# Kernel optimization log

Hardware: AMD Instinct MI355X
Metric: run time of the kernel (lower is better)

Reference implementation:

```python
import jax, jax.numpy as jnp
import numpy as np

D = 256; DFFN = 1024; H = 8; NLVL = 4; NPNT = 4; HD = D // H
BS = 4; NQ = 100; NPTS = 25
SPATIAL = [(128, 128), (64, 64), (32, 32), (16, 16)]
LEN_IN = sum(h * w for h, w in SPATIAL)


def _ln(x, g, b, eps=1e-5):
    m = x.mean(-1, keepdims=True)
    v = ((x - m) ** 2).mean(-1, keepdims=True)
    return (x - m) * jax.lax.rsqrt(v + eps) * g + b


def _mha(q, k, v, w_in, b_in, w_out, b_out):
    # torch nn.MultiheadAttention math, batch-first layout [B,S,D]
    B, Sq, _ = q.shape; Sk = k.shape[1]
    wq, wk, wv = jnp.split(w_in, 3, 0); bq, bk, bv = jnp.split(b_in, 3)
    qh = (q @ wq.T + bq).reshape(B, Sq, H, HD).transpose(0, 2, 1, 3)
    kh = (k @ wk.T + bk).reshape(B, Sk, H, HD).transpose(0, 2, 1, 3)
    vh = (v @ wv.T + bv).reshape(B, Sk, H, HD).transpose(0, 2, 1, 3)
    a = jax.nn.softmax(jnp.einsum('bhqd,bhkd->bhqk', qh, kh) * (1.0 / float(np.sqrt(HD))), -1)
    o = jnp.einsum('bhqk,bhkd->bhqd', a, vh).transpose(0, 2, 1, 3).reshape(B, Sq, D)
    return o @ w_out.T + b_out


def _msdeform(query, ref, src, off_w, off_b, aw_w, aw_b, val_w, val_b, out_w, out_b):
    # MSDeformAttn: per-query multi-level bilinear sampling + weighted aggregation
    bs, Lq, _ = query.shape
    value = (src @ val_w.T + val_b).reshape(bs, LEN_IN, H, HD)
    off = (query @ off_w.T + off_b).reshape(bs, Lq, H, NLVL, NPNT, 2)
    aw = jax.nn.softmax((query @ aw_w.T + aw_b).reshape(bs, Lq, H, NLVL * NPNT), -1)
    aw = aw.reshape(bs, Lq, H, NLVL, NPNT)
    norm = jnp.array([[w, h] for h, w in SPATIAL], jnp.float32)  # (W,H) per level
    loc = ref[:, :, None, :, None, :] + off / norm[None, None, None, :, None, :]
    out = jnp.zeros((bs, H, Lq, HD), query.dtype)
    start = 0
    for l, (hh, ww) in enumerate(SPATIAL):
        v_l = value[:, start:start + hh * ww].transpose(0, 2, 1, 3)  # [bs,H,hw,HD]
        start += hh * ww
        # grid_sample align_corners=False pixel coords: loc*size - 0.5
        x = (loc[:, :, :, l, :, 0] * ww - 0.5).transpose(0, 2, 1, 3).reshape(bs, H, Lq * NPNT)
        y = (loc[:, :, :, l, :, 1] * hh - 0.5).transpose(0, 2, 1, 3).reshape(bs, H, Lq * NPNT)
        x0 = jnp.floor(x); y0 = jnp.floor(y); wx = x - x0; wy = y - y0
        x0i = x0.astype(jnp.int32); y0i = y0.astype(jnp.int32); x1i = x0i + 1; y1i = y0i + 1
        def g(xi, yi):
            valid = ((xi >= 0) & (xi < ww) & (yi >= 0) & (yi < hh)).astype(query.dtype)
            idx = jnp.clip(yi, 0, hh - 1) * ww + jnp.clip(xi, 0, ww - 1)
            return jnp.take_along_axis(v_l, idx[..., None], axis=2) * valid[..., None]
        s = (g(x0i, y0i) * ((1 - wx) * (1 - wy))[..., None]
             + g(x1i, y0i) * (wx * (1 - wy))[..., None]
             + g(x0i, y1i) * ((1 - wx) * wy)[..., None]
             + g(x1i, y1i) * (wx * wy)[..., None])
        s = s.reshape(bs, H, Lq, NPNT, HD)
        out = out + (s * aw[:, :, :, l].transpose(0, 2, 1, 3)[..., None]).sum(3)
    return out.transpose(0, 2, 1, 3).reshape(bs, Lq, D) @ out_w.T + out_b


def _fwd(tgt, query_pos, reference_points, src,
         w_in_intra, b_in_intra, w_out_intra, b_out_intra, g_norm_intra, b_norm_intra,
         w_in_inter, b_in_inter, w_out_inter, b_out_inter, g_norm_inter, b_norm_inter,
         off_w, off_b, aw_w, aw_b, val_w, val_b, co_w, co_b, g_norm_cross, b_norm_cross,
         lin1_w, lin1_b, lin2_w, lin2_b, g_norm3, b_norm3):
    bs, nq, npts, d = tgt.shape
    # intra-instance self-attention (over control points)
    q = (tgt + query_pos).reshape(bs * nq, npts, d)
    t2 = _mha(q, q, tgt.reshape(bs * nq, npts, d), w_in_intra, b_in_intra, w_out_intra, b_out_intra)
    tgt = _ln(tgt + t2.reshape(bs, nq, npts, d), g_norm_intra, b_norm_intra)
    # inter-instance self-attention (over queries), no pos embed per source code
    ti = tgt.transpose(0, 2, 1, 3).reshape(bs * npts, nq, d)
    t2 = _mha(ti, ti, ti, w_in_inter, b_in_inter, w_out_inter, b_out_inter)
    ti = _ln(ti + t2, g_norm_inter, b_norm_inter).reshape(bs, npts, nq, d).transpose(0, 2, 1, 3)
    # deformable cross-attention
    ref = jnp.broadcast_to(reference_points[:, :, None], (bs, nq, npts, NLVL, 2)).reshape(bs, nq * npts, NLVL, 2)
    qc = (ti + query_pos).reshape(bs, nq * npts, d)
    t2 = _msdeform(qc, ref, src, off_w, off_b, aw_w, aw_b, val_w, val_b, co_w, co_b).reshape(bs, nq, npts, d)
    tgt = _ln(ti + t2, g_norm_cross, b_norm_cross)
    # FFN
    ff = jax.nn.relu(tgt @ lin1_w.T + lin1_b) @ lin2_w.T + lin2_b
    return _ln(tgt + ff, g_norm3, b_norm3)


def setup_inputs() -> dict:
    key = jax.random.key(0)
    ki = iter(jax.random.split(key, 40))
    def rn(shape, sc=0.02):
        return jax.random.normal(next(ki), shape, jnp.float32) * sc
    inp = dict(
        tgt=jax.random.normal(next(ki), (BS, NQ, NPTS, D), jnp.float32),
        query_pos=jax.random.normal(next(ki), (BS, NQ, NPTS, D), jnp.float32),
        reference_points=jax.random.uniform(next(ki), (BS, NQ, NLVL, 2), jnp.float32),
        src=jax.random.normal(next(ki), (BS, LEN_IN, D), jnp.float32),
        w_in_intra=rn((3 * D, D)), b_in_intra=jnp.zeros((3 * D,), jnp.float32),
        w_out_intra=rn((D, D)), b_out_intra=jnp.zeros((D,), jnp.float32),
        g_norm_intra=jnp.ones((D,), jnp.float32), b_norm_intra=jnp.zeros((D,), jnp.float32),
        w_in_inter=rn((3 * D, D)), b_in_inter=jnp.zeros((3 * D,), jnp.float32),
        w_out_inter=rn((D, D)), b_out_inter=jnp.zeros((D,), jnp.float32),
        g_norm_inter=jnp.ones((D,), jnp.float32), b_norm_inter=jnp.zeros((D,), jnp.float32),
        off_w=rn((H * NLVL * NPNT * 2, D), 0.001), off_b=rn((H * NLVL * NPNT * 2,), 0.5),
        aw_w=rn((H * NLVL * NPNT, D)), aw_b=jnp.zeros((H * NLVL * NPNT,), jnp.float32),
        val_w=rn((D, D)), val_b=jnp.zeros((D,), jnp.float32),
        co_w=rn((D, D)), co_b=jnp.zeros((D,), jnp.float32),
        g_norm_cross=jnp.ones((D,), jnp.float32), b_norm_cross=jnp.zeros((D,), jnp.float32),
        lin1_w=rn((DFFN, D)), lin1_b=jnp.zeros((DFFN,), jnp.float32),
        lin2_w=rn((D, DFFN)), lin2_b=jnp.zeros((D,), jnp.float32),
        g_norm3=jnp.ones((D,), jnp.float32), b_norm3=jnp.zeros((D,), jnp.float32),
        src_spatial_shapes=jnp.array(SPATIAL, jnp.int32),
        level_start_index=jnp.array(np.cumsum([0] + [h * w for h, w in SPATIAL[:-1]]), jnp.int32),
    )
    return inp


def reference(tgt, query_pos, reference_points, src,
              w_in_intra, b_in_intra, w_out_intra, b_out_intra, g_norm_intra, b_norm_intra,
              w_in_inter, b_in_inter, w_out_inter, b_out_inter, g_norm_inter, b_norm_inter,
              off_w, off_b, aw_w, aw_b, val_w, val_b, co_w, co_b, g_norm_cross, b_norm_cross,
              lin1_w, lin1_b, lin2_w, lin2_b, g_norm3, b_norm3,
              src_spatial_shapes, level_start_index):
    # spatial shapes / level starts are compile-time constants (SPATIAL); args kept for signature parity
    return _fwd(tgt, query_pos, reference_points, src,
                w_in_intra, b_in_intra, w_out_intra, b_out_intra, g_norm_intra, b_norm_intra,
                w_in_inter, b_in_inter, w_out_inter, b_out_inter, g_norm_inter, b_norm_inter,
                off_w, off_b, aw_w, aw_b, val_w, val_b, co_w, co_b, g_norm_cross, b_norm_cross,
                lin1_w, lin1_b, lin2_w, lin2_b, g_norm3, b_norm3)
```

## Files before the change

### kernel.cpp

```cpp
#include <hip/hip_runtime.h>
#include <math.h>

#define DMODEL 256
#define HEADS  8
#define HDIM   32
#define BS     4
#define NQ     100
#define NPTS   25
#define LQ     2500
#define M10K   10000
#define LEN_IN 21760
#define MVAL   87040

typedef float f32x4 __attribute__((ext_vector_type(4)));
typedef short s16x8 __attribute__((ext_vector_type(8)));
typedef unsigned short u16;

static __device__ __forceinline__ short f2bf(float f) {
    unsigned u = __builtin_bit_cast(unsigned, f);
    u = (u + 0x7fffu + ((u >> 16) & 1u)) >> 16;
    return (short)u;
}
static __device__ __forceinline__ unsigned pack2(float lo, float hi) {
    return (unsigned)(u16)f2bf(lo) | ((unsigned)(u16)f2bf(hi) << 16);
}
static __device__ __forceinline__ float bf_lo(unsigned u) {
    return __builtin_bit_cast(float, u << 16);
}
static __device__ __forceinline__ float bf_hi(unsigned u) {
    return __builtin_bit_cast(float, u & 0xffff0000u);
}

#define LDSK   40
#define LDSK64 72

__global__ __launch_bounds__(256) void convert_weights_kernel(
    const float* __restrict__ s0, const float* __restrict__ s1,
    const float* __restrict__ s2, const float* __restrict__ s3,
    const float* __restrict__ s4, const float* __restrict__ s5,
    const float* __restrict__ s6, const float* __restrict__ s7,
    const float* __restrict__ s8, const float* __restrict__ s9,
    u16* __restrict__ dst)
{
    int t8 = (blockIdx.x * 256 + threadIdx.x) * 8;
    if (t8 >= 1277952) return;
    const float* s; int base;
    if      (t8 <  196608) { s = s0; base = 0;       }
    else if (t8 <  262144) { s = s1; base = 196608;  }
    else if (t8 <  458752) { s = s2; base = 262144;  }
    else if (t8 <  524288) { s = s3; base = 458752;  }
    else if (t8 <  589824) { s = s4; base = 524288;  }
    else if (t8 <  622592) { s = s5; base = 589824;  }
    else if (t8 <  688128) { s = s6; base = 622592;  }
    else if (t8 <  753664) { s = s7; base = 688128;  }
    else if (t8 < 1015808) { s = s8; base = 753664;  }
    else                   { s = s9; base = 1015808; }
    const float* p = s + (t8 - base);
    float4 a = *(const float4*)p;
    float4 b = *(const float4*)(p + 4);
    s16x8 v;
    v[0]=f2bf(a.x); v[1]=f2bf(a.y); v[2]=f2bf(a.z); v[3]=f2bf(a.w);
    v[4]=f2bf(b.x); v[5]=f2bf(b.y); v[6]=f2bf(b.z); v[7]=f2bf(b.w);
    *(s16x8*)(dst + t8) = v;
}

__global__ __launch_bounds__(256) void add_convert_kernel(
    const float* __restrict__ a, const float* __restrict__ b,
    u16* __restrict__ xb, u16* __restrict__ ab, int n8)
{
    int i = blockIdx.x * 256 + threadIdx.x;
    if (i >= n8) return;
    size_t o = (size_t)i * 8;
    float4 a0 = *(const float4*)(a + o);
    float4 a1 = *(const float4*)(a + o + 4);
    if (ab) {
        s16x8 v;
        v[0]=f2bf(a0.x); v[1]=f2bf(a0.y); v[2]=f2bf(a0.z); v[3]=f2bf(a0.w);
        v[4]=f2bf(a1.x); v[5]=f2bf(a1.y); v[6]=f2bf(a1.z); v[7]=f2bf(a1.w);
        *(s16x8*)(ab + o) = v;
    }
    if (b) {
        float4 b0 = *(const float4*)(b + o);
        float4 b1 = *(const float4*)(b + o + 4);
        a0.x += b0.x; a0.y += b0.y; a0.z += b0.z; a0.w += b0.w;
        a1.x += b1.x; a1.y += b1.y; a1.z += b1.z; a1.w += b1.w;
    }
    s16x8 v;
    v[0]=f2bf(a0.x); v[1]=f2bf(a0.y); v[2]=f2bf(a0.z); v[3]=f2bf(a0.w);
    v[4]=f2bf(a1.x); v[5]=f2bf(a1.y); v[6]=f2bf(a1.z); v[7]=f2bf(a1.w);
    *(s16x8*)(xb + o) = v;
}

__global__ __launch_bounds__(256) void gemm_mfma_kernel(
    const u16* __restrict__ A, int lda,
    const u16* __restrict__ W, int K,
    const float* __restrict__ bias,
    void* __restrict__ Cv, int ldc,
    int M, int relu, int out_bf16)
{
    __shared__ short As[64 * LDSK64];
    __shared__ short Ws[64 * LDSK64];

    const int tid = threadIdx.x;
    const int m0 = blockIdx.y * 64, n0 = blockIdx.x * 64;
    const int srow = tid >> 2;
    const int sk = (tid & 3) * 16;
    const int wave = tid >> 6;
    const int wm = wave & 1, wn = wave >> 1;
    const int lane = tid & 63;
    const int lrow = lane & 15;
    const int kq = lane >> 4;

    const int gm = m0 + srow;
    const u16* aptr = A + (size_t)gm * lda + sk;
    const u16* wptr = W + (size_t)(n0 + srow) * K + sk;

    f32x4 acc[2][2];
#pragma unroll
    for (int i = 0; i < 2; ++i)
#pragma unroll
        for (int j = 0; j < 2; ++j) acc[i][j] = (f32x4)(0.f);

    s16x8 a0 = (s16x8)0, a1 = (s16x8)0, w0, w1;
    if (gm < M) { a0 = *(const s16x8*)aptr; a1 = *(const s16x8*)(aptr + 8); }
    w0 = *(const s16x8*)wptr; w1 = *(const s16x8*)(wptr + 8);

    for (int k0 = 0; k0 < K; k0 += 64) {
        *(s16x8*)&As[srow * LDSK64 + sk]     = a0;
        *(s16x8*)&As[srow * LDSK64 + sk + 8] = a1;
        *(s16x8*)&Ws[srow * LDSK64 + sk]     = w0;
        *(s16x8*)&Ws[srow * LDSK64 + sk + 8] = w1;
        __syncthreads();
        if (k0 + 64 < K) {
            if (gm < M) {
                a0 = *(const s16x8*)(aptr + k0 + 64);
                a1 = *(const s16x8*)(aptr + k0 + 72);
            }
            w0 = *(const s16x8*)(wptr + k0 + 64);
            w1 = *(const s16x8*)(wptr + k0 + 72);
        }

#pragma unroll
        for (int s = 0; s < 2; ++s) {
            s16x8 af[2], bfv[2];
#pragma unroll
            for (int i = 0; i < 2; ++i)
                af[i] = *(const s16x8*)&As[(wm * 32 + i * 16 + lrow) * LDSK64 + s * 32 + kq * 8];
#pragma unroll
            for (int j = 0; j < 2; ++j)
                bfv[j] = *(const s16x8*)&Ws[(wn * 32 + j * 16 + lrow) * LDSK64 + s * 32 + kq * 8];
#pragma unroll
            for (int i = 0; i < 2; ++i)
#pragma unroll
                for (int j = 0; j < 2; ++j)
                    acc[i][j] = __builtin_amdgcn_mfma_f32_16x16x32_bf16(af[i], bfv[j], acc[i][j], 0, 0, 0);
        }
        __syncthreads();
    }

#pragma unroll
    for (int i = 0; i < 2; ++i)
#pragma unroll
        for (int j = 0; j < 2; ++j) {
            int col = n0 + wn * 32 + j * 16 + lrow;
            float bv = bias[col];
#pragma unroll
            for (int reg = 0; reg < 4; ++reg) {
                int gmo = m0 + wm * 32 + i * 16 + kq * 4 + reg;
                if (gmo < M) {
                    float v = acc[i][j][reg] + bv;
                    if (relu) v = fmaxf(v, 0.f);
                    if (out_bf16)
                        ((u16*)Cv)[(size_t)gmo * ldc + col] = (u16)f2bf(v);
                    else
                        ((float*)Cv)[(size_t)gmo * ldc + col] = v;
                }
            }
        }
}

__global__ __launch_bounds__(256) void gemm_mfma128_kernel(
    const u16* __restrict__ A, int lda,
    const u16* __restrict__ W, int K,
    const float* __restrict__ bias,
    void* __restrict__ Cv, int ldc,
    int M, int relu, int out_bf16)
{
    __shared__ short As[128 * LDSK];
    __shared__ short Ws[128 * LDSK];

    const int tid = threadIdx.x;
    const int m0 = blockIdx.y * 128, n0 = blockIdx.x * 128;

    const int srow = tid >> 1;
    const int sk = (tid & 1) * 16;

    const int wave = tid >> 6;
    const int wm = wave & 1, wn = wave >> 1;
    const int lane = tid & 63;
    const int lrow = lane & 15;
    const int kq = lane >> 4;

    const int gm = m0 + srow;
    const u16* aptr = A + (size_t)gm * lda + sk;
    const u16* wptr = W + (size_t)(n0 + srow) * K + sk;

    f32x4 acc[4][4];
#pragma unroll
    for (int i = 0; i < 4; ++i)
#pragma unroll
        for (int j = 0; j < 4; ++j) acc[i][j] = (f32x4)(0.f);

    s16x8 a0 = (s16x8)0, a1 = (s16x8)0, w0, w1;
    if (gm < M) { a0 = *(const s16x8*)aptr; a1 = *(const s16x8*)(aptr + 8); }
    w0 = *(const s16x8*)wptr; w1 = *(const s16x8*)(wptr + 8);

    for (int k0 = 0; k0 < K; k0 += 32) {
        *(s16x8*)&As[srow * LDSK + sk]     = a0;
        *(s16x8*)&As[srow * LDSK + sk + 8] = a1;
        *(s16x8*)&Ws[srow * LDSK + sk]     = w0;
        *(s16x8*)&Ws[srow * LDSK + sk + 8] = w1;
        __syncthreads();
        if (k0 + 32 < K) {
            if (gm < M) {
                a0 = *(const s16x8*)(aptr + k0 + 32);
                a1 = *(const s16x8*)(aptr + k0 + 40);
            }
            w0 = *(const s16x8*)(wptr + k0 + 32);
            w1 = *(const s16x8*)(wptr + k0 + 40);
        }

        s16x8 af[4], bfv[4];
#pragma unroll
        for (int i = 0; i < 4; ++i)
            af[i] = *(const s16x8*)&As[(wm * 64 + i * 16 + lrow) * LDSK + kq * 8];
#pragma unroll
        for (int j = 0; j < 4; ++j)
            bfv[j] = *(const s16x8*)&Ws[(wn * 64 + j * 16 + lrow) * LDSK + kq * 8];
#pragma unroll
        for (int i = 0; i < 4; ++i)
#pragma unroll
            for (int j = 0; j < 4; ++j)
                acc[i][j] = __builtin_amdgcn_mfma_f32_16x16x32_bf16(af[i], bfv[j], acc[i][j], 0, 0, 0);
        __syncthreads();
    }

#pragma unroll
    for (int i = 0; i < 4; ++i)
#pragma unroll
        for (int j = 0; j < 4; ++j) {
            int col = n0 + wn * 64 + j * 16 + lrow;
            float bv = bias[col];
#pragma unroll
            for (int reg = 0; reg < 4; ++reg) {
                int gmo = m0 + wm * 64 + i * 16 + kq * 4 + reg;
                if (gmo < M) {
                    float v = acc[i][j][reg] + bv;
                    if (relu) v = fmaxf(v, 0.f);
                    if (out_bf16)
                        ((u16*)Cv)[(size_t)gmo * ldc + col] = (u16)f2bf(v);
                    else
                        ((float*)Cv)[(size_t)gmo * ldc + col] = v;
                }
            }
        }
}

__global__ __launch_bounds__(256) void gemm_value128_kernel(
    const float* __restrict__ A,
    const u16* __restrict__ W,
    const float* __restrict__ bias,
    u16* __restrict__ C, int M)
{
    __shared__ short As[128 * LDSK];
    __shared__ short Ws[128 * LDSK];

    const int tid = threadIdx.x;
    const int m0 = blockIdx.y * 128, n0 = blockIdx.x * 128;

    const int srow = tid >> 1;
    const int sk = (tid & 1) * 16;

    const int wave = tid >> 6;
    const int wm = wave & 1, wn = wave >> 1;
    const int lane = tid & 63;
    const int lrow = lane & 15;
    const int kq = lane >> 4;

    const int gm = m0 + srow;
    const float* aptr = A + (size_t)gm * 256 + sk;
    const u16* wptr = W + (size_t)(n0 + srow) * 256 + sk;

    f32x4 acc[4][4];
#pragma unroll
    for (int i = 0; i < 4; ++i)
#pragma unroll
        for (int j = 0; j < 4; ++j) acc[i][j] = (f32x4)(0.f);

    float4 pa[4];
    s16x8 w0, w1;
#pragma unroll
    for (int t = 0; t < 4; ++t) pa[t] = make_float4(0.f, 0.f, 0.f, 0.f);
    if (gm < M) {
#pragma unroll
        for (int t = 0; t < 4; ++t) pa[t] = *(const float4*)(aptr + t * 4);
    }
    w0 = *(const s16x8*)wptr; w1 = *(const s16x8*)(wptr + 8);

    for (int k0 = 0; k0 < 256; k0 += 32) {
        s16x8 av0, av1;
        av0[0]=f2bf(pa[0].x); av0[1]=f2bf(pa[0].y); av0[2]=f2bf(pa[0].z); av0[3]=f2bf(pa[0].w);
        av0[4]=f2bf(pa[1].x); av0[5]=f2bf(pa[1].y); av0[6]=f2bf(pa[1].z); av0[7]=f2bf(pa[1].w);
        av1[0]=f2bf(pa[2].x); av1[1]=f2bf(pa[2].y); av1[2]=f2bf(pa[2].z); av1[3]=f2bf(pa[2].w);
        av1[4]=f2bf(pa[3].x); av1[5]=f2bf(pa[3].y); av1[6]=f2bf(pa[3].z); av1[7]=f2bf(pa[3].w);
        *(s16x8*)&As[srow * LDSK + sk]     = av0;
        *(s16x8*)&As[srow * LDSK + sk + 8] = av1;
        *(s16x8*)&Ws[srow * LDSK + sk]     = w0;
        *(s16x8*)&Ws[srow * LDSK + sk + 8] = w1;
        __syncthreads();
        if (k0 + 32 < 256) {
            if (gm < M) {
#pragma unroll
                for (int t = 0; t < 4; ++t)
                    pa[t] = *(const float4*)(aptr + k0 + 32 + t * 4);
            }
            w0 = *(const s16x8*)(wptr + k0 + 32);
            w1 = *(const s16x8*)(wptr + k0 + 40);
        }

        s16x8 af[4], bfv[4];
#pragma unroll
        for (int i = 0; i < 4; ++i)
            af[i] = *(const s16x8*)&As[(wm * 64 + i * 16 + lrow) * LDSK + kq * 8];
#pragma unroll
        for (int j = 0; j < 4; ++j)
            bfv[j] = *(const s16x8*)&Ws[(wn * 64 + j * 16 + lrow) * LDSK + kq * 8];
#pragma unroll
        for (int i = 0; i < 4; ++i)
#pragma unroll
            for (int j = 0; j < 4; ++j)
                acc[i][j] = __builtin_amdgcn_mfma_f32_16x16x32_bf16(af[i], bfv[j], acc[i][j], 0, 0, 0);
        __syncthreads();
    }

#pragma unroll
    for (int i = 0; i < 4; ++i)
#pragma unroll
        for (int j = 0; j < 4; ++j) {
            int col = n0 + wn * 64 + j * 16 + lrow;
            float bv = bias[col];
#pragma unroll
            for (int reg = 0; reg < 4; ++reg) {
                int gmo = m0 + wm * 64 + i * 16 + kq * 4 + reg;
                if (gmo < M)
                    C[(size_t)gmo * 256 + col] = (u16)f2bf(acc[i][j][reg] + bv);
            }
        }
}

__global__ __launch_bounds__(256) void inter_attn_mfma_kernel(
    const float* __restrict__ qkv, u16* __restrict__ out, float scale)
{
    __shared__ __align__(16) u16 Qs[112 * 40];
    __shared__ __align__(16) u16 Ks[112 * 40];
    __shared__ __align__(16) u16 Vt[32 * 136];
    __shared__ __align__(16) u16 Ps[112 * 136];

    const int b = blockIdx.x, h = blockIdx.y;
    const float* base = qkv + (size_t)b * 100 * 768;
    const int tid = threadIdx.x;
    const int wave = tid >> 6, lane = tid & 63;
    const int lr = lane & 15, quad = lane >> 4;

    for (int i = tid; i < 12 * 20; i += 256) {
        int row = 100 + i / 20, c = (i % 20) * 2;
        *(unsigned*)&Qs[row * 40 + c] = 0;
        *(unsigned*)&Ks[row * 40 + c] = 0;
    }
    for (int i = tid; i < 2176; i += 256) ((unsigned*)Vt)[i] = 0;
    for (int i = tid; i < 7616; i += 256) ((unsigned*)Ps)[i] = 0;
    __syncthreads();

    for (int idx = tid; idx < 2400; idx += 256) {
        int row = idx / 24, s = idx % 24;
        const float* p = (s < 8)  ? base + row * 768 + h * 32 + s * 4
                       : (s < 16) ? base + row * 768 + 256 + h * 32 + (s - 8) * 4
                                  : base + row * 768 + 512 + h * 32 + (s - 16) * 4;
        float4 f = *(const float4*)p;
        if (s < 8) {
            unsigned* q = (unsigned*)&Qs[row * 40 + s * 4];
            q[0] = pack2(f.x, f.y); q[1] = pack2(f.z, f.w);
        } else if (s < 16) {
            unsigned* q = (unsigned*)&Ks[row * 40 + (s - 8) * 4];
            q[0] = pack2(f.x, f.y); q[1] = pack2(f.z, f.w);
        } else {
            int d0 = (s - 16) * 4;
            Vt[(d0 + 0) * 136 + row] = (u16)f2bf(f.x);
            Vt[(d0 + 1) * 136 + row] = (u16)f2bf(f.y);
            Vt[(d0 + 2) * 136 + row] = (u16)f2bf(f.z);
            Vt[(d0 + 3) * 136 + row] = (u16)f2bf(f.w);
        }
    }
    __syncthreads();

#pragma unroll 1
    for (int rr = 0; rr < 2; ++rr) {
        int rt = wave + rr * 4;
        if (rt < 7) {
            s16x8 aq = *(const s16x8*)&Qs[(rt * 16 + lr) * 40 + quad * 8];
            f32x4 sc[7];
#pragma unroll
            for (int ct = 0; ct < 7; ++ct) {
                s16x8 bk = *(const s16x8*)&Ks[(ct * 16 + lr) * 40 + quad * 8];
                sc[ct] = __builtin_amdgcn_mfma_f32_16x16x32_bf16(aq, bk, (f32x4)(0.f), 0, 0, 0);
            }
            const bool colok[7] = {true, true, true, true, true, true, (lr < 4)};
#pragma unroll
            for (int reg = 0; reg < 4; ++reg) {
                float mx = -1e30f;
#pragma unroll
                for (int ct = 0; ct < 7; ++ct) {
                    float sv = sc[ct][reg] * scale;
                    sc[ct][reg] = sv;
                    if (colok[ct]) mx = fmaxf(mx, sv);
                }
#pragma unroll
                for (int d = 1; d < 16; d <<= 1) mx = fmaxf(mx, __shfl_xor(mx, d));
                float ssum = 0.f;
#pragma unroll
                for (int ct = 0; ct < 7; ++ct) {
                    float pv = colok[ct] ? __expf(sc[ct][reg] - mx) : 0.f;
                    sc[ct][reg] = pv;
                    ssum += pv;
                }
#pragma unroll
                for (int d = 1; d < 16; d <<= 1) ssum += __shfl_xor(ssum, d);
                float inv = 1.f / ssum;
                int prow = rt * 16 + quad * 4 + reg;
#pragma unroll
                for (int ct = 0; ct < 7; ++ct)
                    Ps[prow * 136 + ct * 16 + lr] = (u16)f2bf(sc[ct][reg] * inv);
            }
        }
    }
    __syncthreads();

#pragma unroll 1
    for (int rr = 0; rr < 2; ++rr) {
        int rt = wave + rr * 4;
        if (rt < 7) {
            f32x4 o0 = (f32x4)(0.f), o1 = (f32x4)(0.f);
#pragma unroll
            for (int kk = 0; kk < 4; ++kk) {
                s16x8 ap = *(const s16x8*)&Ps[(rt * 16 + lr) * 136 + kk * 32 + quad * 8];
                s16x8 bv0 = *(const s16x8*)&Vt[lr * 136 + kk * 32 + quad * 8];
                s16x8 bv1 = *(const s16x8*)&Vt[(16 + lr) * 136 + kk * 32 + quad * 8];
                o0 = __builtin_amdgcn_mfma_f32_16x16x32_bf16(ap, bv0, o0, 0, 0, 0);
                o1 = __builtin_amdgcn_mfma_f32_16x16x32_bf16(ap, bv1, o1, 0, 0, 0);
            }
#pragma unroll
            for (int reg = 0; reg < 4; ++reg) {
                int q = rt * 16 + quad * 4 + reg;
                if (q < 100) {
                    u16* op = out + ((size_t)b * 100 + q) * 256 + h * 32;
                    op[lr]      = (u16)f2bf(o0[reg]);
                    op[16 + lr] = (u16)f2bf(o1[reg]);
                }
            }
        }
    }
}

__global__ __launch_bounds__(256) void intra_attn_kernel(
    const float* __restrict__ qkv, u16* __restrict__ out, float scale)
{
    __shared__ float4 KV[25][128];

    const int b = blockIdx.x;
    const int h = threadIdx.x >> 5, r = threadIdx.x & 31;
    const float* base = qkv + (size_t)b * 25 * 768;

    for (int idx = threadIdx.x; idx < 3200; idx += 256) {
        int row = idx >> 7, c = idx & 127;
        KV[row][c] = *(const float4*)(base + row * 768 + 256 + c * 4);
    }

    float q[32];
    if (r < 25) {
        const float* qp = base + r * 768 + h * 32;
#pragma unroll
        for (int c4 = 0; c4 < 8; ++c4) {
            float4 f = *(const float4*)(qp + c4 * 4);
            q[c4*4+0] = f.x; q[c4*4+1] = f.y; q[c4*4+2] = f.z; q[c4*4+3] = f.w;
        }
    }
    __syncthreads();

    if (r < 25) {
        float m = -1e30f, l = 0.f, acc[32];
#pragma unroll
        for (int c = 0; c < 32; ++c) acc[c] = 0.f;
#pragma unroll 2
        for (int j = 0; j < 25; ++j) {
            const float4* kr = &KV[j][h * 8];
            float dot = 0.f;
#pragma unroll
            for (int c4 = 0; c4 < 8; ++c4) {
                float4 kf = kr[c4];
                dot = fmaf(q[c4*4+0], kf.x, dot);
                dot = fmaf(q[c4*4+1], kf.y, dot);
                dot = fmaf(q[c4*4+2], kf.z, dot);
                dot = fmaf(q[c4*4+3], kf.w, dot);
            }
            dot *= scale;
            float mn = fmaxf(m, dot);
            float alpha = __expf(m - mn);
            float p = __expf(dot - mn);
            l = l * alpha + p;
            const float4* vr = &KV[j][64 + h * 8];
#pragma unroll
            for (int c4 = 0; c4 < 8; ++c4) {
                float4 vf = vr[c4];
                acc[c4*4+0] = acc[c4*4+0] * alpha + p * vf.x;
                acc[c4*4+1] = acc[c4*4+1] * alpha + p * vf.y;
                acc[c4*4+2] = acc[c4*4+2] * alpha + p * vf.z;
                acc[c4*4+3] = acc[c4*4+3] * alpha + p * vf.w;
            }
            m = mn;
        }
        float inv = 1.f / l;
        unsigned* op = (unsigned*)(out + ((size_t)b * 25 + r) * 256 + h * 32);
#pragma unroll
        for (int c = 0; c < 16; ++c)
            op[c] = pack2(acc[2*c] * inv, acc[2*c+1] * inv);
    }
}

__global__ __launch_bounds__(64) void add_ln_kernel(
    const float* __restrict__ a, const float* __restrict__ b,
    const float* __restrict__ g, const float* __restrict__ beta,
    float* __restrict__ out, u16* __restrict__ out_bf, int transpose_mode)
{
    const int r = blockIdx.x;
    const int lane = threadIdx.x;
    const float* ar = a + (size_t)r * 256;
    const float* br = b + (size_t)r * 256;
    float x[4];
    float s = 0.f;
#pragma unroll
    for (int i = 0; i < 4; ++i) {
        x[i] = ar[lane + 64 * i] + br[lane + 64 * i];
        s += x[i];
    }
#pragma unroll
    for (int off = 32; off >= 1; off >>= 1) s += __shfl_xor(s, off);
    float mean = s * (1.f / 256.f);
    float vs = 0.f;
#pragma unroll
    for (int i = 0; i < 4; ++i) { float d = x[i] - mean; vs += d * d; }
#pragma unroll
    for (int off = 32; off >= 1; off >>= 1) vs += __shfl_xor(vs, off);
    float rstd = rsqrtf(vs * (1.f / 256.f) + 1e-5f);

    size_t ro = r;
    if (transpose_mode) {
        int q = r % 100; int bp = r / 100; int p = bp % 25; int bb = bp / 25;
        ro = ((size_t)bb * 100 + q) * 25 + p;
    }
    float* orow = out + ro * 256;
    u16* brow = out_bf ? out_bf + ro * 256 : (u16*)0;
#pragma unroll
    for (int i = 0; i < 4; ++i) {
        int c = lane + 64 * i;
        float v = (x[i] - mean) * rstd * g[c] + beta[c];
        orow[c] = v;
        if (brow) brow[c] = (u16)f2bf(v);
    }
}

__global__ __launch_bounds__(64) void tgt_to_ti_kernel(
    const float* __restrict__ tgt1, float* __restrict__ ti, u16* __restrict__ tib)
{
    const int r = blockIdx.x;
    int q = r % 100; int bp = r / 100; int p = bp % 25; int b = bp / 25;
    const float4* srcp = (const float4*)(tgt1 + (((size_t)b * 100 + q) * 25 + p) * 256);
    float4 v = srcp[threadIdx.x];
    ((float4*)(ti + (size_t)r * 256))[threadIdx.x] = v;
    uint2 pk = make_uint2(pack2(v.x, v.y), pack2(v.z, v.w));
    ((uint2*)(tib + (size_t)r * 256))[threadIdx.x] = pk;
}

__global__ __launch_bounds__(256, 4) void msdeform_sample_kernel(
    const u16* __restrict__ value,
    const float* __restrict__ off,
    const float* __restrict__ awl,
    const float* __restrict__ refp,
    u16* __restrict__ sampled)
{
    const int unit = blockIdx.x * 8 + (threadIdx.x >> 5);
    const int t = threadIdx.x & 31;
    const int h = t >> 2, c8 = t & 3;
    const int b = unit / LQ, lq = unit - b * LQ;
    const int q = lq / NPTS;

    const float* awp = awl + (size_t)unit * 128 + h * 16;
    float w[16];
    float mx = -1e30f;
#pragma unroll
    for (int k = 0; k < 16; ++k) { w[k] = awp[k]; mx = fmaxf(mx, w[k]); }
    float sum = 0.f;
#pragma unroll
    for (int k = 0; k < 16; ++k) { w[k] = __expf(w[k] - mx); sum += w[k]; }
    const float inv = 1.f / sum;

    const float* offp = off + (size_t)unit * 256 + h * 32;
    const float* rp = refp + ((size_t)b * 100 + q) * 8;
    const u16* vbase = value + (size_t)b * LEN_IN * 256 + h * 32 + c8 * 8;

    float acc[8];
#pragma unroll
    for (int k = 0; k < 8; ++k) acc[k] = 0.f;

    int start = 0;
    const int sz[4] = {128, 64, 32, 16};
#pragma unroll
    for (int l = 0; l < 4; ++l) {
        const int hh = sz[l], ww = sz[l];
        const float rx = rp[l * 2 + 0], ry = rp[l * 2 + 1];
#pragma unroll 1
        for (int pt = 0; pt < 4; ++pt) {
            float ox = offp[(l * 4 + pt) * 2 + 0];
            float oy = offp[(l * 4 + pt) * 2 + 1];
            float x = rx * ww + ox - 0.5f;
            float y = ry * hh + oy - 0.5f;
            float x0f = floorf(x), y0f = floorf(y);
            float wx = x - x0f, wy = y - y0f;
            int x0 = (int)x0f, y0 = (int)y0f;
            int x1 = x0 + 1, y1 = y0 + 1;
            float aw = w[l * 4 + pt] * inv;

            int x0c = min(max(x0, 0), ww - 1), x1c = min(max(x1, 0), ww - 1);
            int y0c = min(max(y0, 0), hh - 1), y1c = min(max(y1, 0), hh - 1);
            float w00 = aw * (1.f - wx) * (1.f - wy);
            float w10 = aw * wx * (1.f - wy);
            float w01 = aw * (1.f - wx) * wy;
            float w11 = aw * wx * wy;
            if (!(x0 >= 0 && x0 < ww)) { w00 = 0.f; w01 = 0.f; }
            if (!(x1 >= 0 && x1 < ww)) { w10 = 0.f; w11 = 0.f; }
            if (!(y0 >= 0 && y0 < hh)) { w00 = 0.f; w10 = 0.f; }
            if (!(y1 >= 0 && y1 < hh)) { w01 = 0.f; w11 = 0.f; }

            uint4 u00 = *(const uint4*)(vbase + (size_t)(start + y0c * ww + x0c) * 256);
            uint4 u10 = *(const uint4*)(vbase + (size_t)(start + y0c * ww + x1c) * 256);
            uint4 u01 = *(const uint4*)(vbase + (size_t)(start + y1c * ww + x0c) * 256);
            uint4 u11 = *(const uint4*)(vbase + (size_t)(start + y1c * ww + x1c) * 256);

#define ACC4(u, wgt) \
            acc[0] = fmaf(wgt, bf_lo(u.x), acc[0]); \
            acc[1] = fmaf(wgt, bf_hi(u.x), acc[1]); \
            acc[2] = fmaf(wgt, bf_lo(u.y), acc[2]); \
            acc[3] = fmaf(wgt, bf_hi(u.y), acc[3]); \
            acc[4] = fmaf(wgt, bf_lo(u.z), acc[4]); \
            acc[5] = fmaf(wgt, bf_hi(u.z), acc[5]); \
            acc[6] = fmaf(wgt, bf_lo(u.w), acc[6]); \
            acc[7] = fmaf(wgt, bf_hi(u.w), acc[7]);
            ACC4(u00, w00); ACC4(u10, w10); ACC4(u01, w01); ACC4(u11, w11);
#undef ACC4
        }
        start += hh * ww;
    }

    uint4 pk;
    pk.x = pack2(acc[0], acc[1]); pk.y = pack2(acc[2], acc[3]);
    pk.z = pack2(acc[4], acc[5]); pk.w = pack2(acc[6], acc[7]);
    *(uint4*)(sampled + (size_t)unit * 256 + h * 32 + c8 * 8) = pk;
}

extern "C" void kernel_launch(void* const* d_in, const int* in_sizes, int n_in,
                              void* d_out, int out_size, void* d_ws, size_t ws_size,
                              hipStream_t stream)
{
    (void)in_sizes; (void)n_in; (void)out_size; (void)ws_size;

    const float* tgt        = (const float*)d_in[0];
    const float* query_pos  = (const float*)d_in[1];
    const float* refp       = (const float*)d_in[2];
    const float* src        = (const float*)d_in[3];
    const float* w_in_intra = (const float*)d_in[4];
    const float* b_in_intra = (const float*)d_in[5];
    const float* w_out_intra= (const float*)d_in[6];
    const float* b_out_intra= (const float*)d_in[7];
    const float* g_ln_intra = (const float*)d_in[8];
    const float* b_ln_intra = (const float*)d_in[9];
    const float* w_in_inter = (const float*)d_in[10];
    const float* b_in_inter = (const float*)d_in[11];
    const float* w_out_inter= (const float*)d_in[12];
    const float* b_out_inter= (const float*)d_in[13];
    const float* g_ln_inter = (const float*)d_in[14];
    const float* b_ln_inter = (const float*)d_in[15];
    const float* off_w      = (const float*)d_in[16];
    const float* off_b      = (const float*)d_in[17];
    const float* aw_w       = (const float*)d_in[18];
    const float* aw_b       = (const float*)d_in[19];
    const float* val_w      = (const float*)d_in[20];
    const float* val_b      = (const float*)d_in[21];
    const float* co_w       = (const float*)d_in[22];
    const float* co_b       = (const float*)d_in[23];
    const float* g_ln_cross = (const float*)d_in[24];
    const float* b_ln_cross = (const float*)d_in[25];
    const float* lin1_w     = (const float*)d_in[26];
    const float* lin1_b     = (const float*)d_in[27];
    const float* lin2_w     = (const float*)d_in[28];
    const float* lin2_b     = (const float*)d_in[29];
    const float* g_ln3      = (const float*)d_in[30];
    const float* b_ln3      = (const float*)d_in[31];

    float* ws    = (float*)d_ws;
    float* qkv   = ws;
    float* tmp   = ws + 7680000;
    u16*   attnb = (u16*)(ws + 10240000);
    float* tgt1  = ws + 11520000;
    float* ti    = ws + 14080000;
    u16*   tib   = (u16*)(ws + 16640000);
    float* tA    = ws + 17920000;
    u16*   qcb   = (u16*)(ws + 20480000);
    u16*   x1b   = (u16*)(ws + 21760000);
    u16*   tgtb  = (u16*)(ws + 23040000);
    float* awl   = ws + 24320000;
    u16*   valueb= (u16*)(ws + 25600000);
    u16*   wb    = (u16*)(ws + 36741120);
    float* out   = (float*)d_out;

    u16* wb_in_intra  = wb;
    u16* wb_out_intra = wb + 196608;
    u16* wb_in_inter  = wb + 262144;
    u16* wb_out_inter = wb + 458752;
    u16* wb_off       = wb + 524288;
    u16* wb_aw        = wb + 589824;
    u16* wb_val       = wb + 622592;
    u16* wb_co        = wb + 688128;
    u16* wb_lin1      = wb + 753664;
    u16* wb_lin2      = wb + 1015808;

    const float scale = 0.17677669529663687f;
    const int MB64  = (M10K + 63) / 64;
    const int MB128 = (M10K + 127) / 128;

    convert_weights_kernel<<<624, 256, 0, stream>>>(
        w_in_intra, w_out_intra, w_in_inter, w_out_inter, off_w,
        aw_w, val_w, co_w, lin1_w, lin2_w, wb);
    add_convert_kernel<<<1250, 256, 0, stream>>>(tgt, query_pos, x1b, tgtb, 320000);

    gemm_mfma128_kernel<<<dim3(4, MB128), 256, 0, stream>>>(x1b, 256, wb_in_intra, 256,
                                                            b_in_intra, qkv, 768, M10K, 0, 0);
    gemm_mfma_kernel<<<dim3(4, MB64), 256, 0, stream>>>(tgtb, 256, wb_in_intra + 512 * 256, 256,
                                                        b_in_intra + 512, qkv + 512, 768, M10K, 0, 0);
    intra_attn_kernel<<<400, 256, 0, stream>>>(qkv, attnb, scale);
    gemm_mfma_kernel<<<dim3(4, MB64), 256, 0, stream>>>(attnb, 256, wb_out_intra, 256,
                                                        b_out_intra, tmp, 256, M10K, 0, 0);
    add_ln_kernel<<<M10K, 64, 0, stream>>>(tgt, tmp, g_ln_intra, b_ln_intra, tgt1, (u16*)0, 0);

    tgt_to_ti_kernel<<<M10K, 64, 0, stream>>>(tgt1, ti, tib);
    gemm_mfma128_kernel<<<dim3(6, MB128), 256, 0, stream>>>(tib, 256, wb_in_inter, 256,
                                                            b_in_inter, qkv, 768, M10K, 0, 0);
    inter_attn_mfma_kernel<<<dim3(100, 8), 256, 0, stream>>>(qkv, attnb, scale);
    gemm_mfma_kernel<<<dim3(4, MB64), 256, 0, stream>>>(attnb, 256, wb_out_inter, 256,
                                                        b_out_inter, tmp, 256, M10K, 0, 0);
    add_ln_kernel<<<M10K, 64, 0, stream>>>(ti, tmp, g_ln_inter, b_ln_inter, tA, (u16*)0, 1);

    add_convert_kernel<<<1250, 256, 0, stream>>>(tA, query_pos, qcb, (u16*)0, 320000);
    gemm_value128_kernel<<<dim3(2, 680), 256, 0, stream>>>(src, wb_val, val_b, valueb, MVAL);
    gemm_mfma_kernel<<<dim3(4, MB64), 256, 0, stream>>>(qcb, 256, wb_off, 256,
                                                        off_b, tgt1, 256, M10K, 0, 0);
    gemm_mfma_kernel<<<dim3(2, MB64), 256, 0, stream>>>(qcb, 256, wb_aw, 256,
                                                        aw_b, awl, 128, M10K, 0, 0);
    msdeform_sample_kernel<<<1250, 256, 0, stream>>>(valueb, tgt1, awl, refp, attnb);
    gemm_mfma_kernel<<<dim3(4, MB64), 256, 0, stream>>>(attnb, 256, wb_co, 256,
                                                        co_b, tmp, 256, M10K, 0, 0);
    add_ln_kernel<<<M10K, 64, 0, stream>>>(tA, tmp, g_ln_cross, b_ln_cross, ti, tib, 0);

    gemm_mfma128_kernel<<<dim3(8, MB128), 256, 0, stream>>>(tib, 256, wb_lin1, 256,
                                                            lin1_b, valueb, 1024, M10K, 1, 1);
    gemm_mfma_kernel<<<dim3(4, MB64), 256, 0, stream>>>(valueb, 1024, wb_lin2, 1024,
                                                        lin2_b, tmp, 256, M10K, 0, 0);
    add_ln_kernel<<<M10K, 64, 0, stream>>>(ti, tmp, g_ln3, b_ln3, out, (u16*)0, 0);
}
```

Baseline: 471.7 us.

## Keep value-projection weight tile resident in LDS and stream A from registers

Replaces the value-projection GEMM with a kernel that loads the full 128x256 bf16 weight slice into LDS once per block, then has each wave stream its own 64 rows of fp32 source directly into registers, converting them to bf16 MFMA A-fragments with no LDS staging. A chunks are double-buffered in registers and per-k-step syncthreads are removed, and each block now covers 256 rows. The aim is to drop repeated weight reloads and barrier overhead in this memory-bound GEMM. It uses heavy register pressure (two 8x2 float4 buffers), relies on M being a multiple of 256 since the bounds check is dropped, and A loads are no longer coalesced through LDS.

```diff
diff --git a/kernel.cpp b/kernel.cpp
--- a/kernel.cpp
+++ b/kernel.cpp
@@ -33,6 +33,7 @@
 
 #define LDSK   40
 #define LDSK64 72
+#define LDSW   264
 
 __global__ __launch_bounds__(256) void convert_weights_kernel(
     const float* __restrict__ s0, const float* __restrict__ s1,
@@ -266,96 +267,89 @@
         }
 }
 
-__global__ __launch_bounds__(256) void gemm_value128_kernel(
+static __device__ __forceinline__ void vload_chunk(const float* p, float4 (&buf)[8][2]) {
+#pragma unroll
+    for (int s = 0; s < 8; ++s) {
+        buf[s][0] = *(const float4*)(p + s * 32);
+        buf[s][1] = *(const float4*)(p + s * 32 + 4);
+    }
+}
+static __device__ __forceinline__ void vcvt_chunk(const float4 (&buf)[8][2], s16x8 (&a)[8]) {
+#pragma unroll
+    for (int s = 0; s < 8; ++s) {
+        a[s][0] = f2bf(buf[s][0].x); a[s][1] = f2bf(buf[s][0].y);
+        a[s][2] = f2bf(buf[s][0].z); a[s][3] = f2bf(buf[s][0].w);
+        a[s][4] = f2bf(buf[s][1].x); a[s][5] = f2bf(buf[s][1].y);
+        a[s][6] = f2bf(buf[s][1].z); a[s][7] = f2bf(buf[s][1].w);
+    }
+}
+
+__global__ __launch_bounds__(256, 2) void gemm_value_wres_kernel(
     const float* __restrict__ A,
     const u16* __restrict__ W,
     const float* __restrict__ bias,
-    u16* __restrict__ C, int M)
-{
-    __shared__ short As[128 * LDSK];
-    __shared__ short Ws[128 * LDSK];
+    u16* __restrict__ C)
+{
+    __shared__ __align__(16) u16 Wl[128 * LDSW];
 
     const int tid = threadIdx.x;
-    const int m0 = blockIdx.y * 128, n0 = blockIdx.x * 128;
-
-    const int srow = tid >> 1;
-    const int sk = (tid & 1) * 16;
-
-    const int wave = tid >> 6;
-    const int wm = wave & 1, wn = wave >> 1;
-    const int lane = tid & 63;
-    const int lrow = lane & 15;
-    const int kq = lane >> 4;
-
-    const int gm = m0 + srow;
-    const float* aptr = A + (size_t)gm * 256 + sk;
-    const u16* wptr = W + (size_t)(n0 + srow) * 256 + sk;
-
-    f32x4 acc[4][4];
-#pragma unroll
-    for (int i = 0; i < 4; ++i)
-#pragma unroll
-        for (int j = 0; j < 4; ++j) acc[i][j] = (f32x4)(0.f);
-
-    float4 pa[4];
-    s16x8 w0, w1;
-#pragma unroll
-    for (int t = 0; t < 4; ++t) pa[t] = make_float4(0.f, 0.f, 0.f, 0.f);
-    if (gm < M) {
-#pragma unroll
-        for (int t = 0; t < 4; ++t) pa[t] = *(const float4*)(aptr + t * 4);
-    }
-    w0 = *(const s16x8*)wptr; w1 = *(const s16x8*)(wptr + 8);
-
-    for (int k0 = 0; k0 < 256; k0 += 32) {
-        s16x8 av0, av1;
-        av0[0]=f2bf(pa[0].x); av0[1]=f2bf(pa[0].y); av0[2]=f2bf(pa[0].z); av0[3]=f2bf(pa[0].w);
-        av0[4]=f2bf(pa[1].x); av0[5]=f2bf(pa[1].y); av0[6]=f2bf(pa[1].z); av0[7]=f2bf(pa[1].w);
-        av1[0]=f2bf(pa[2].x); av1[1]=f2bf(pa[2].y); av1[2]=f2bf(pa[2].z); av1[3]=f2bf(pa[2].w);
-        av1[4]=f2bf(pa[3].x); av1[5]=f2bf(pa[3].y); av1[6]=f2bf(pa[3].z); av1[7]=f2bf(pa[3].w);
-        *(s16x8*)&As[srow * LDSK + sk]     = av0;
-        *(s16x8*)&As[srow * LDSK + sk + 8] = av1;
-        *(s16x8*)&Ws[srow * LDSK + sk]     = w0;
-        *(s16x8*)&Ws[srow * LDSK + sk + 8] = w1;
-        __syncthreads();
-        if (k0 + 32 < 256) {
-            if (gm < M) {
-#pragma unroll
-                for (int t = 0; t < 4; ++t)
-                    pa[t] = *(const float4*)(aptr + k0 + 32 + t * 4);
-            }
-            w0 = *(const s16x8*)(wptr + k0 + 32);
-            w1 = *(const s16x8*)(wptr + k0 + 40);
-        }
-
-        s16x8 af[4], bfv[4];
-#pragma unroll
-        for (int i = 0; i < 4; ++i)
-            af[i] = *(const s16x8*)&As[(wm * 64 + i * 16 + lrow) * LDSK + kq * 8];
-#pragma unroll
-        for (int j = 0; j < 4; ++j)
-            bfv[j] = *(const s16x8*)&Ws[(wn * 64 + j * 16 + lrow) * LDSK + kq * 8];
-#pragma unroll
-        for (int i = 0; i < 4; ++i)
-#pragma unroll
-            for (int j = 0; j < 4; ++j)
-                acc[i][j] = __builtin_amdgcn_mfma_f32_16x16x32_bf16(af[i], bfv[j], acc[i][j], 0, 0, 0);
-        __syncthreads();
-    }
-
-#pragma unroll
-    for (int i = 0; i < 4; ++i)
-#pragma unroll
-        for (int j = 0; j < 4; ++j) {
-            int col = n0 + wn * 64 + j * 16 + lrow;
-            float bv = bias[col];
-#pragma unroll
-            for (int reg = 0; reg < 4; ++reg) {
-                int gmo = m0 + wm * 64 + i * 16 + kq * 4 + reg;
-                if (gmo < M)
-                    C[(size_t)gmo * 256 + col] = (u16)f2bf(acc[i][j][reg] + bv);
-            }
-        }
+    const int n0 = blockIdx.x * 128;
+    const int m0 = blockIdx.y * 256;
+
+    {
+        const int row = tid >> 1, half = tid & 1;
+        const u16* src = W + (size_t)(n0 + row) * 256 + half * 128;
+        u16* dst = &Wl[row * LDSW + half * 128];
+#pragma unroll
+        for (int i = 0; i < 16; ++i)
+            *(uint4*)(dst + i * 8) = *(const uint4*)(src + i * 8);
+    }
+    __syncthreads();
+
+    const int wave = tid >> 6, lane = tid & 63;
+    const int lrow = lane & 15, kq = lane >> 4;
+
+    float bv[8];
+#pragma unroll
+    for (int j = 0; j < 8; ++j) bv[j] = bias[n0 + j * 16 + lrow];
+
+    const int rbase = m0 + wave * 64;
+    const float* aptr = A + (size_t)(rbase + lrow) * 256 + kq * 8;
+
+    float4 pa[8][2], pb[8][2];
+    vload_chunk(aptr, pa);
+
+#pragma unroll
+    for (int c = 0; c < 4; ++c) {
+        if (c < 3) {
+            const float* np = aptr + (c + 1) * 16 * 256;
+            if (c & 1) vload_chunk(np, pa);
+            else       vload_chunk(np, pb);
+        }
+
+        s16x8 a[8];
+        if (c & 1) vcvt_chunk(pb, a);
+        else       vcvt_chunk(pa, a);
+
+        f32x4 acc[8];
+#pragma unroll
+        for (int j = 0; j < 8; ++j) acc[j] = (f32x4)(0.f);
+#pragma unroll
+        for (int s = 0; s < 8; ++s)
+#pragma unroll
+            for (int j = 0; j < 8; ++j) {
+                s16x8 bfv = *(const s16x8*)&Wl[(j * 16 + lrow) * LDSW + s * 32 + kq * 8];
+                acc[j] = __builtin_amdgcn_mfma_f32_16x16x32_bf16(a[s], bfv, acc[j], 0, 0, 0);
+            }
+
+        const int grow = rbase + c * 16 + kq * 4;
+        u16* crow = C + (size_t)grow * 256 + n0 + lrow;
+#pragma unroll
+        for (int j = 0; j < 8; ++j)
+#pragma unroll
+            for (int reg = 0; reg < 4; ++reg)
+                crow[(size_t)reg * 256 + j * 16] = (u16)f2bf(acc[j][reg] + bv[j]);
+    }
 }
 
 __global__ __launch_bounds__(256) void inter_attn_mfma_kernel(
@@ -769,7 +763,7 @@
     add_ln_kernel<<<M10K, 64, 0, stream>>>(ti, tmp, g_ln_inter, b_ln_inter, tA, (u16*)0, 1);
 
     add_convert_kernel<<<1250, 256, 0, stream>>>(tA, query_pos, qcb, (u16*)0, 320000);
-    gemm_value128_kernel<<<dim3(2, 680), 256, 0, stream>>>(src, wb_val, val_b, valueb, MVAL);
+    gemm_value_wres_kernel<<<dim3(2, 340), 256, 0, stream>>>(src, wb_val, val_b, valueb);
     gemm_mfma_kernel<<<dim3(4, MB64), 256, 0, stream>>>(qcb, 256, wb_off, 256,
                                                         off_b, tgt1, 256, M10K, 0, 0);
     gemm_mfma_kernel<<<dim3(2, MB64), 256, 0, stream>>>(qcb, 256, wb_aw, 256,
```

After: 470.1 us. Within noise of the previous version (-0.3%).
